# Kernel optimization log

Measured on AMD Instinct MI355X. Metric: run time of the kernel, lower is better.

The kernel has to match this reference:

```python
import jax, jax.numpy as jnp
import numpy as np

PASSES = 5
NUM_EDGE_SETS = 3
B, N, D = 8, 20000, 128
E = 64000
HID, OUT = 80, 10


def setup_inputs() -> dict:
    key = jax.random.key(0)
    ks = jax.random.split(key, 8)
    nodes = jax.random.normal(ks[0], (B, N, D), dtype=jnp.float32)
    problem_type = jax.random.normal(ks[1], (B, 1), dtype=jnp.float32)
    # edges[b, k, e] = (dst, src); index_add target is column 0, gathered source is column 1
    edges = jax.random.randint(ks[2], (B, NUM_EDGE_SETS, E, 2), 0, N, dtype=jnp.int32)
    w1 = jax.random.normal(ks[3], (D + 1, HID), jnp.float32) / np.sqrt(D + 1).astype(np.float32)
    b1 = jnp.zeros((HID,), jnp.float32)
    w2 = jax.random.normal(ks[4], (HID, HID), jnp.float32) / np.sqrt(HID).astype(np.float32)
    b2 = jnp.zeros((HID,), jnp.float32)
    w3 = jax.random.normal(ks[5], (HID, OUT), jnp.float32) / np.sqrt(HID).astype(np.float32)
    b3 = jnp.zeros((OUT,), jnp.float32)
    return {"nodes": nodes, "problem_type": problem_type, "w1": w1, "b1": b1,
            "w2": w2, "b2": b2, "w3": w3, "b3": b3, "edges": edges}


def _message_pass(nodes_g, edges_g):
    # nodes_g: [N, D]; edges_g: [K, E, 2] with (dst, src)
    inc = jnp.zeros_like(nodes_g)
    for k in range(NUM_EDGE_SETS):  # small fixed set of edge types
        dst = edges_g[k, :, 0]
        src = edges_g[k, :, 1]
        inc = inc + jax.ops.segment_sum(nodes_g[src], dst, num_segments=N)
    return nodes_g + inc


def _forward(nodes, problem_type, w1, b1, w2, b2, w3, b3, edges):
    step = jax.vmap(_message_pass)  # over batch of graphs

    def body(n, _):
        return step(n, edges), None

    nodes, _ = jax.lax.scan(body, nodes, None, length=PASSES)
    pooled = nodes.sum(axis=1)                       # [B, D]
    y = jnp.log(pooled)
    y = jnp.where(jnp.isnan(y), 0.0, y)              # nan -> 0
    y = jax.nn.relu(y)
    finite_max = jnp.max(jnp.where(jnp.isinf(y), -jnp.inf, y), axis=1, keepdims=True)
    y = jnp.where(y == jnp.inf, finite_max, y)       # +inf -> max finite entry
    x = jnp.concatenate([y, problem_type], axis=1)   # [B, D+1]
    x = jax.nn.leaky_relu(x @ w1 + b1)
    x = jax.nn.leaky_relu(x @ w2 + b2)
    return x @ w3 + b3                               # [B, OUT]


def reference(nodes, problem_type, w1, b1, w2, b2, w3, b3, edges):
    return _forward(nodes, problem_type, w1, b1, w2, b2, w3, b3, edges)
```

## Files before the change

### kernel.cpp

```cpp
#include <hip/hip_runtime.h>
#include <cmath>

#define NB 8
#define NN 20000
#define ND 128
#define NE_TOT 192000

#define RSZ 128
#define NR 157
#define CAP 2048
#define ECHUNK 8000
#define NCHUNK 24

__device__ float g_w0[NB * NN];
__device__ float g_w1[NB * NN];
__device__ int   g_bcnt[NB][NCHUNK][NR];
__device__ int   g_cnt[NB * NR];
__device__ int2  g_bucket[(size_t)NB * NR * CAP];
__device__ float g_ppart[(size_t)NB * NR * ND];

__global__ void initCountK(const int* __restrict__ edges) {
    __shared__ int hist[NR];
    const int b = blockIdx.x / NCHUNK, c = blockIdx.x % NCHUNK;
    const int t = threadIdx.x;

    for (int i = blockIdx.x * 256 + t; i < NB * NN; i += NB * NCHUNK * 256)
        g_w0[i] = 1.0f;

    for (int i = t; i < NR; i += 256) hist[i] = 0;
    __syncthreads();
    const int2* __restrict__ ep =
        (const int2*)edges + (size_t)b * NE_TOT + (size_t)c * ECHUNK;
    for (int i = t; i < ECHUNK; i += 256)
        atomicAdd(&hist[ep[i].y >> 7], 1);
    __syncthreads();
    for (int i = t; i < NR; i += 256) g_bcnt[b][c][i] = hist[i];
}

__global__ void distK(const int* __restrict__ edges) {
    __shared__ int cur[NR];
    const int b = blockIdx.x / NCHUNK, c = blockIdx.x % NCHUNK;
    const int t = threadIdx.x;
    for (int r = t; r < NR; r += 256) {
        int off = 0;
        for (int cc = 0; cc < c; ++cc) off += g_bcnt[b][cc][r];
        cur[r] = off;
        if (c == NCHUNK - 1) g_cnt[b * NR + r] = off + g_bcnt[b][c][r];
    }
    __syncthreads();
    const int2* __restrict__ ep =
        (const int2*)edges + (size_t)b * NE_TOT + (size_t)c * ECHUNK;
    for (int i = t; i < ECHUNK; i += 256) {
        const int2 e = ep[i];
        const int r = e.y >> 7;
        const int pos = atomicAdd(&cur[r], 1);
        if (pos < CAP)
            g_bucket[((size_t)b * NR + r) * CAP + pos] = make_int2(e.x, e.y & (RSZ - 1));
    }
}

__global__ void passK(int sel) {
    __shared__ float acc[RSZ];
    const int b = blockIdx.x / NR, r = blockIdx.x % NR;
    const int t = threadIdx.x;
    const float* __restrict__ w  = sel ? g_w1 : g_w0;
    float* __restrict__ wn       = sel ? g_w0 : g_w1;
    if (t < RSZ) acc[t] = 0.0f;
    __syncthreads();
    const int cnt = g_cnt[b * NR + r];
    const int2* __restrict__ bk = g_bucket + ((size_t)b * NR + r) * CAP;
    const float* __restrict__ wb = w + b * NN;
    for (int i = t; i < cnt; i += 256) {
        const int2 e = bk[i];
        unsafeAtomicAdd(&acc[e.y], wb[e.x]);
    }
    __syncthreads();
    const int node = (r << 7) + t;
    if (t < RSZ && node < NN)
        wn[b * NN + node] = wb[node] + acc[t];
}

__global__ void pass5poolK(const float* __restrict__ nodes) {
    __shared__ float acc[RSZ];
    __shared__ float w5s[RSZ];
    __shared__ __align__(16) float4 red[256];
    const int b = blockIdx.x / NR, r = blockIdx.x % NR;
    const int t = threadIdx.x;
    const float* __restrict__ wb = g_w0 + b * NN;

    if (t < RSZ) acc[t] = 0.0f;
    __syncthreads();
    const int cnt = g_cnt[b * NR + r];
    const int2* __restrict__ bk = g_bucket + ((size_t)b * NR + r) * CAP;
    for (int i = t; i < cnt; i += 256) {
        const int2 e = bk[i];
        unsafeAtomicAdd(&acc[e.y], wb[e.x]);
    }
    __syncthreads();
    if (t < RSZ) {
        const int node = (r << 7) + t;
        w5s[t] = (node < NN) ? wb[node] + acc[t] : 0.0f;
    }
    __syncthreads();

    const int dslot = t & 31, rg = t >> 5;
    const float4* __restrict__ base = (const float4*)(nodes + (size_t)b * NN * ND);
    const int nbase = r << 7;
    float4 a[4];
    a[0] = a[1] = a[2] = a[3] = make_float4(0.f, 0.f, 0.f, 0.f);
#pragma unroll
    for (int k = 0; k < 16; ++k) {
        const int nl = rg + (k << 3);
        const int node = nbase + nl;
        if (node < NN) {
            const float wv = w5s[nl];
            const float4 v = base[(size_t)node * 32 + dslot];
            a[k & 3].x += wv * v.x; a[k & 3].y += wv * v.y;
            a[k & 3].z += wv * v.z; a[k & 3].w += wv * v.w;
        }
    }
    float4 s4;
    s4.x = (a[0].x + a[1].x) + (a[2].x + a[3].x);
    s4.y = (a[0].y + a[1].y) + (a[2].y + a[3].y);
    s4.z = (a[0].z + a[1].z) + (a[2].z + a[3].z);
    s4.w = (a[0].w + a[1].w) + (a[2].w + a[3].w);
    red[t] = s4;
    __syncthreads();
    if (t < 32) {
        float4 s = red[t];
        for (int g = 1; g < 8; ++g) {
            const float4 o = red[g * 32 + t];
            s.x += o.x; s.y += o.y; s.z += o.z; s.w += o.w;
        }
        ((float4*)g_ppart)[((size_t)b * NR + r) * 32 + t] = s;
    }
}

__global__ void reduceHeadK(const float* __restrict__ ptype,
                            const float* __restrict__ w1, const float* __restrict__ b1,
                            const float* __restrict__ w2, const float* __restrict__ b2,
                            const float* __restrict__ w3, const float* __restrict__ b3,
                            float* __restrict__ out) {
    __shared__ float sx[NB][ND + 1];
    __shared__ float h1s[NB][80];
    __shared__ float h2s[NB][80];
    const int t = threadIdx.x;
    const int b = t >> 7, d = t & 127;

    float s = 0.0f;
    for (int r = 0; r < NR; ++r)
        s += g_ppart[(((size_t)b * NR + r) << 7) + d];

    float y = logf(s);
    if (isnan(y)) y = 0.0f;
    y = fmaxf(y, 0.0f);
    sx[b][d] = y;
    __syncthreads();

    if (t < NB) {
        float fm = -INFINITY;
        for (int dd = 0; dd < ND; ++dd) {
            const float v = sx[t][dd];
            if (!isinf(v)) fm = fmaxf(fm, v);
        }
        for (int dd = 0; dd < ND; ++dd)
            if (isinf(sx[t][dd])) sx[t][dd] = fm;
        sx[t][ND] = ptype[t];
    }
    __syncthreads();

    if (t < NB * 80) {
        const int bb = t / 80, j = t - bb * 80;
        float v = b1[j];
        for (int k = 0; k < ND + 1; ++k) v += sx[bb][k] * w1[k * 80 + j];
        h1s[bb][j] = v > 0.0f ? v : 0.01f * v;
    }
    __syncthreads();

    if (t < NB * 80) {
        const int bb = t / 80, j = t - bb * 80;
        float v = b2[j];
        for (int k = 0; k < 80; ++k) v += h1s[bb][k] * w2[k * 80 + j];
        h2s[bb][j] = v > 0.0f ? v : 0.01f * v;
    }
    __syncthreads();

    if (t < NB * 10) {
        const int bb = t / 10, j = t - bb * 10;
        float v = b3[j];
        for (int k = 0; k < 80; ++k) v += h2s[bb][k] * w3[k * 10 + j];
        out[bb * 10 + j] = v;
    }
}

extern "C" void kernel_launch(void* const* d_in, const int* in_sizes, int n_in,
                              void* d_out, int out_size, void* d_ws, size_t ws_size,
                              hipStream_t stream) {
    const float* nodes = (const float*)d_in[0];
    const float* ptype = (const float*)d_in[1];
    const float* w1    = (const float*)d_in[2];
    const float* b1    = (const float*)d_in[3];
    const float* w2    = (const float*)d_in[4];
    const float* b2    = (const float*)d_in[5];
    const float* w3    = (const float*)d_in[6];
    const float* b3    = (const float*)d_in[7];
    const int*   edges = (const int*)d_in[8];
    float* out = (float*)d_out;

    initCountK<<<NB * NCHUNK, 256, 0, stream>>>(edges);
    distK<<<NB * NCHUNK, 256, 0, stream>>>(edges);

    passK<<<NB * NR, 256, 0, stream>>>(0);
    passK<<<NB * NR, 256, 0, stream>>>(1);
    passK<<<NB * NR, 256, 0, stream>>>(0);
    passK<<<NB * NR, 256, 0, stream>>>(1);

    pass5poolK<<<NB * NR, 256, 0, stream>>>(nodes);

    reduceHeadK<<<1, 1024, 0, stream>>>(ptype, w1, b1, w2, b2, w3, b3, out);
}
```

Before: 132.7 us.

## Stage per-graph node weights in LDS and group five row buckets per block

Each pass block now copies the whole per-graph weight vector (20000 floats) into LDS, then processes five 128-node row buckets with 1024 threads. Random gathers of source weights hit LDS instead of global memory or L2. The pool kernel is restructured the same way, and the partial-sum count per graph drops from 157 to 32, which shortens the final reduction. The trade-off is that each block redundantly loads 80 KB, occupancy is limited to one large block per CU, and the grid shrinks to 256 blocks.

```diff
diff --git a/kernel.cpp b/kernel.cpp
--- a/kernel.cpp
+++ b/kernel.cpp
@@ -12,12 +12,15 @@
 #define ECHUNK 8000
 #define NCHUNK 24
 
+#define GR 5
+#define NCG 32
+
 __device__ float g_w0[NB * NN];
 __device__ float g_w1[NB * NN];
 __device__ int   g_bcnt[NB][NCHUNK][NR];
 __device__ int   g_cnt[NB * NR];
 __device__ int2  g_bucket[(size_t)NB * NR * CAP];
-__device__ float g_ppart[(size_t)NB * NR * ND];
+__device__ float g_ppart[NB * NCG * ND];
 
 __global__ void initCountK(const int* __restrict__ edges) {
     __shared__ int hist[NR];
@@ -59,80 +62,107 @@
     }
 }
 
-__global__ void passK(int sel) {
-    __shared__ float acc[RSZ];
-    const int b = blockIdx.x / NR, r = blockIdx.x % NR;
-    const int t = threadIdx.x;
+__global__ void __launch_bounds__(1024)
+passLDSK(int sel) {
+    extern __shared__ float w_lds[];
+    __shared__ float acc[GR * RSZ];
+    const int b  = blockIdx.y;
+    const int r0 = blockIdx.x * GR;
+    const int gr = min(GR, NR - r0);
+    const int t  = threadIdx.x;
     const float* __restrict__ w  = sel ? g_w1 : g_w0;
     float* __restrict__ wn       = sel ? g_w0 : g_w1;
-    if (t < RSZ) acc[t] = 0.0f;
-    __syncthreads();
-    const int cnt = g_cnt[b * NR + r];
-    const int2* __restrict__ bk = g_bucket + ((size_t)b * NR + r) * CAP;
     const float* __restrict__ wb = w + b * NN;
-    for (int i = t; i < cnt; i += 256) {
-        const int2 e = bk[i];
-        unsafeAtomicAdd(&acc[e.y], wb[e.x]);
-    }
-    __syncthreads();
-    const int node = (r << 7) + t;
-    if (t < RSZ && node < NN)
-        wn[b * NN + node] = wb[node] + acc[t];
-}
-
-__global__ void pass5poolK(const float* __restrict__ nodes) {
-    __shared__ float acc[RSZ];
-    __shared__ float w5s[RSZ];
-    __shared__ __align__(16) float4 red[256];
-    const int b = blockIdx.x / NR, r = blockIdx.x % NR;
-    const int t = threadIdx.x;
+
+    const float4* __restrict__ wb4 = (const float4*)wb;
+    for (int i = t; i < NN / 4; i += 1024) ((float4*)w_lds)[i] = wb4[i];
+    if (t < GR * RSZ) acc[t] = 0.0f;
+    __syncthreads();
+
+    for (int rr = 0; rr < gr; ++rr) {
+        const int u = b * NR + r0 + rr;
+        const int cnt = g_cnt[u];
+        const int2* __restrict__ bk = g_bucket + (size_t)u * CAP;
+        float* accr = acc + rr * RSZ;
+        for (int i = t; i < cnt; i += 1024) {
+            const int2 e = bk[i];
+            unsafeAtomicAdd(&accr[e.y], w_lds[e.x]);
+        }
+    }
+    __syncthreads();
+
+    for (int i = t; i < gr * RSZ; i += 1024) {
+        const int node = r0 * RSZ + i;
+        if (node < NN) wn[b * NN + node] = w_lds[node] + acc[i];
+    }
+}
+
+__global__ void __launch_bounds__(1024)
+pass5poolK(const float* __restrict__ nodes) {
+    extern __shared__ float w_lds[];
+    __shared__ float acc[GR * RSZ];
+    __shared__ float w5s[GR * RSZ];
+    const int b  = blockIdx.y;
+    const int r0 = blockIdx.x * GR;
+    const int gr = min(GR, NR - r0);
+    const int t  = threadIdx.x;
     const float* __restrict__ wb = g_w0 + b * NN;
 
-    if (t < RSZ) acc[t] = 0.0f;
-    __syncthreads();
-    const int cnt = g_cnt[b * NR + r];
-    const int2* __restrict__ bk = g_bucket + ((size_t)b * NR + r) * CAP;
-    for (int i = t; i < cnt; i += 256) {
-        const int2 e = bk[i];
-        unsafeAtomicAdd(&acc[e.y], wb[e.x]);
-    }
-    __syncthreads();
-    if (t < RSZ) {
-        const int node = (r << 7) + t;
-        w5s[t] = (node < NN) ? wb[node] + acc[t] : 0.0f;
+    const float4* __restrict__ wb4 = (const float4*)wb;
+    for (int i = t; i < NN / 4; i += 1024) ((float4*)w_lds)[i] = wb4[i];
+    if (t < GR * RSZ) acc[t] = 0.0f;
+    __syncthreads();
+
+    for (int rr = 0; rr < gr; ++rr) {
+        const int u = b * NR + r0 + rr;
+        const int cnt = g_cnt[u];
+        const int2* __restrict__ bk = g_bucket + (size_t)u * CAP;
+        float* accr = acc + rr * RSZ;
+        for (int i = t; i < cnt; i += 1024) {
+            const int2 e = bk[i];
+            unsafeAtomicAdd(&accr[e.y], w_lds[e.x]);
+        }
+    }
+    __syncthreads();
+
+    if (t < GR * RSZ) {
+        const int node = r0 * RSZ + t;
+        w5s[t] = (t < gr * RSZ && node < NN) ? w_lds[node] + acc[t] : 0.0f;
     }
     __syncthreads();
 
     const int dslot = t & 31, rg = t >> 5;
+    const int nbase = r0 * RSZ;
+    const int nrows = min(GR * RSZ, NN - nbase);
     const float4* __restrict__ base = (const float4*)(nodes + (size_t)b * NN * ND);
-    const int nbase = r << 7;
-    float4 a[4];
-    a[0] = a[1] = a[2] = a[3] = make_float4(0.f, 0.f, 0.f, 0.f);
-#pragma unroll
-    for (int k = 0; k < 16; ++k) {
-        const int nl = rg + (k << 3);
-        const int node = nbase + nl;
-        if (node < NN) {
-            const float wv = w5s[nl];
-            const float4 v = base[(size_t)node * 32 + dslot];
-            a[k & 3].x += wv * v.x; a[k & 3].y += wv * v.y;
-            a[k & 3].z += wv * v.z; a[k & 3].w += wv * v.w;
-        }
+    float4 aA = {0.f, 0.f, 0.f, 0.f}, aB = {0.f, 0.f, 0.f, 0.f};
+    int row = rg;
+    for (; row + 32 < nrows; row += 64) {
+        const float wA = w5s[row], wB = w5s[row + 32];
+        const float4 vA = base[(size_t)(nbase + row) * 32 + dslot];
+        const float4 vB = base[(size_t)(nbase + row + 32) * 32 + dslot];
+        aA.x += wA * vA.x; aA.y += wA * vA.y; aA.z += wA * vA.z; aA.w += wA * vA.w;
+        aB.x += wB * vB.x; aB.y += wB * vB.y; aB.z += wB * vB.z; aB.w += wB * vB.w;
+    }
+    if (row < nrows) {
+        const float wA = w5s[row];
+        const float4 vA = base[(size_t)(nbase + row) * 32 + dslot];
+        aA.x += wA * vA.x; aA.y += wA * vA.y; aA.z += wA * vA.z; aA.w += wA * vA.w;
     }
     float4 s4;
-    s4.x = (a[0].x + a[1].x) + (a[2].x + a[3].x);
-    s4.y = (a[0].y + a[1].y) + (a[2].y + a[3].y);
-    s4.z = (a[0].z + a[1].z) + (a[2].z + a[3].z);
-    s4.w = (a[0].w + a[1].w) + (a[2].w + a[3].w);
+    s4.x = aA.x + aB.x; s4.y = aA.y + aB.y; s4.z = aA.z + aB.z; s4.w = aA.w + aB.w;
+
+    __syncthreads();
+    float4* red = (float4*)w_lds;
     red[t] = s4;
     __syncthreads();
     if (t < 32) {
         float4 s = red[t];
-        for (int g = 1; g < 8; ++g) {
+        for (int g = 1; g < 32; ++g) {
             const float4 o = red[g * 32 + t];
             s.x += o.x; s.y += o.y; s.z += o.z; s.w += o.w;
         }
-        ((float4*)g_ppart)[((size_t)b * NR + r) * 32 + t] = s;
+        ((float4*)g_ppart)[((size_t)b * NCG + blockIdx.x) * 32 + t] = s;
     }
 }
 
@@ -148,8 +178,8 @@
     const int b = t >> 7, d = t & 127;
 
     float s = 0.0f;
-    for (int r = 0; r < NR; ++r)
-        s += g_ppart[(((size_t)b * NR + r) << 7) + d];
+    for (int j = 0; j < NCG; ++j)
+        s += g_ppart[(b * NCG + j) * ND + d];
 
     float y = logf(s);
     if (isnan(y)) y = 0.0f;
@@ -210,12 +240,12 @@
     initCountK<<<NB * NCHUNK, 256, 0, stream>>>(edges);
     distK<<<NB * NCHUNK, 256, 0, stream>>>(edges);
 
-    passK<<<NB * NR, 256, 0, stream>>>(0);
-    passK<<<NB * NR, 256, 0, stream>>>(1);
-    passK<<<NB * NR, 256, 0, stream>>>(0);
-    passK<<<NB * NR, 256, 0, stream>>>(1);
-
-    pass5poolK<<<NB * NR, 256, 0, stream>>>(nodes);
+    passLDSK<<<dim3(NCG, NB), 1024, NN * sizeof(float), stream>>>(0);
+    passLDSK<<<dim3(NCG, NB), 1024, NN * sizeof(float), stream>>>(1);
+    passLDSK<<<dim3(NCG, NB), 1024, NN * sizeof(float), stream>>>(0);
+    passLDSK<<<dim3(NCG, NB), 1024, NN * sizeof(float), stream>>>(1);
+
+    pass5poolK<<<dim3(NCG, NB), 1024, NN * sizeof(float), stream>>>(nodes);
 
     reduceHeadK<<<1, 1024, 0, stream>>>(ptype, w1, b1, w2, b2, w3, b3, out);
 }
```

Result: faster. 129.7 us (-2.3%).
